# Optimization experiments

Measured on AMD Instinct MI355X. Metric: run time of the kernel, lower is better.

The kernel has to match this reference:

```python
import jax, jax.numpy as jnp
import numpy as np

B, L, D = 4096, 50, 64
NU, NI, NR = 100000, 100000, 5


def setup_inputs() -> dict:
    key = jax.random.key(0)
    ks = jax.random.split(key, 16)
    s = 0.02
    inp = {
        "nodes_v": jax.random.randint(ks[0], (B,), 0, NI),
        "neigh_u": jax.random.randint(ks[1], (B, L), 0, NU),
        "neigh_r": jax.random.randint(ks[2], (B, L), 0, NR),
        "embed_u": jax.random.normal(ks[3], (NU, D)) * s,
        "embed_i": jax.random.normal(ks[4], (NI, D)) * s,
        "embed_r": jax.random.normal(ks[5], (NR, D)) * s,
        # gv MLP: Linear(2D,D) ReLU Linear(D,D) ReLU Linear(D,D)
        "gv_w1": jax.random.normal(ks[6], (2 * D, D)) * s, "gv_b1": jnp.zeros((D,)),
        "gv_w2": jax.random.normal(ks[7], (D, D)) * s,     "gv_b2": jnp.zeros((D,)),
        "gv_w3": jax.random.normal(ks[8], (D, D)) * s,     "gv_b3": jnp.zeros((D,)),
        # attention MLP: Linear(2D,D) ReLU Linear(D,D) ReLU Linear(D,1), softmax over neighbors
        "att_w1": jax.random.normal(ks[9], (2 * D, D)) * s, "att_b1": jnp.zeros((D,)),
        "att_w2": jax.random.normal(ks[10], (D, D)) * s,    "att_b2": jnp.zeros((D,)),
        "att_w3": jax.random.normal(ks[11], (D, 1)) * s,    "att_b3": jnp.zeros((1,)),
        # combine: Linear(2D,D) ReLU Linear(D,D) ReLU
        "wr1_w": jax.random.normal(ks[12], (2 * D, D)) * s, "wr1_b": jnp.zeros((D,)),
        "wr2_w": jax.random.normal(ks[13], (D, D)) * s,     "wr2_b": jnp.zeros((D,)),
    }
    return inp


def reference(nodes_v, neigh_u, neigh_r, embed_u, embed_i, embed_r,
              gv_w1, gv_b1, gv_w2, gv_b2, gv_w3, gv_b3,
              att_w1, att_b1, att_w2, att_b2, att_w3, att_b3,
              wr1_w, wr1_b, wr2_w, wr2_b):
    qj = embed_i[nodes_v]            # [B, D] item reps
    pt = embed_u[neigh_u]            # [B, L, D] neighbor user reps
    er = embed_r[neigh_r]            # [B, L, D] rating reps
    # fusion MLP g(.)
    x = jnp.concatenate([pt, er], axis=-1)                    # [B, L, 2D]
    h = jax.nn.relu(x @ gv_w1 + gv_b1)
    h = jax.nn.relu(h @ gv_w2 + gv_b2)
    fjt = h @ gv_w3 + gv_b3                                   # [B, L, D]
    # attention over neighbors (dropout is identity in eval mode)
    q_rep = jnp.broadcast_to(qj[:, None, :], fjt.shape)       # [B, L, D]
    a = jnp.concatenate([fjt, q_rep], axis=-1)                # [B, L, 2D]
    a = jax.nn.relu(a @ att_w1 + att_b1)
    a = jax.nn.relu(a @ att_w2 + att_b2)
    scores = (a @ att_w3 + att_b3)[..., 0]                    # [B, L]
    mu = jax.nn.softmax(scores, axis=1)                       # softmax over neighbors
    zj = jnp.einsum("bld,bl->bd", fjt, mu)                   # weighted aggregation
    # combine aggregated neighborhood with item's own embedding (2D -> D)
    z = jax.nn.relu(jnp.concatenate([zj, qj], axis=-1) @ wr1_w + wr1_b)
    out = jax.nn.relu(z @ wr2_w + wr2_b)                      # [B, D]
    return out
```

## Files before the change

kernel.cpp:

```cpp
#include <hip/hip_runtime.h>

typedef __bf16 bf16;
typedef short s16x8 __attribute__((ext_vector_type(8)));
typedef __bf16 b16x8 __attribute__((ext_vector_type(8)));
typedef float f32x4 __attribute__((ext_vector_type(4)));

#define B_   4096
#define L_   50
#define SH   72

#define OFF_W1F  0
#define OFF_W2F  8192
#define OFF_W3F  12288
#define OFF_WCF  16384
#define OFF_A2F  20480
#define OFF_R1T  24576
#define OFF_R2T  32768
#define WT_TOTAL 36864
#define BIAS1P_BYTE 73728
#define CQ_BYTE     73984

#define PREP_W_BLOCKS 145
#define PREP_C_BLOCKS 1024

__device__ __forceinline__ unsigned short f2b(float f) {
    __bf16 h = (__bf16)f;
    return __builtin_bit_cast(unsigned short, h);
}
__device__ __forceinline__ unsigned pack2(float a, float b) {
    return (unsigned)f2b(a) | ((unsigned)f2b(b) << 16);
}
__device__ __forceinline__ s16x8 mkfrag(float4 a, float4 b) {
    union { s16x8 v; unsigned u[4]; } r;
    r.u[0] = pack2(a.x, a.y); r.u[1] = pack2(a.z, a.w);
    r.u[2] = pack2(b.x, b.y); r.u[3] = pack2(b.z, b.w);
    return r.v;
}
__device__ __forceinline__ f32x4 mfma16(s16x8 a, s16x8 b, f32x4 c) {
    return __builtin_amdgcn_mfma_f32_16x16x32_bf16(a, b, c, 0, 0, 0);
}

template<bool RELU>
__device__ __forceinline__ void dual_layer_lds(const bf16* A0, const bf16* A1,
                                               const bf16* __restrict__ Wf,
                                               const float* __restrict__ bias,
                                               bf16* O0, bf16* O1, int lane)
{
    const int m = lane & 15, quad = lane >> 4;
    f32x4 ac0[4] = {}, ac1[4] = {};
#pragma unroll
    for (int kt = 0; kt < 2; ++kt) {
        s16x8 a0 = *(const s16x8*)(A0 + m * SH + kt * 32 + quad * 8);
        s16x8 a1 = *(const s16x8*)(A1 + m * SH + kt * 32 + quad * 8);
#pragma unroll
        for (int nt = 0; nt < 4; ++nt) {
            s16x8 b = *(const s16x8*)(Wf + (kt * 4 + nt) * 512 + lane * 8);
            ac0[nt] = mfma16(a0, b, ac0[nt]);
            ac1[nt] = mfma16(a1, b, ac1[nt]);
        }
    }
#pragma unroll
    for (int nt = 0; nt < 4; ++nt) {
        int c = nt * 16 + m;
        float bv = bias[c];
#pragma unroll
        for (int r4 = 0; r4 < 4; ++r4) {
            float v0 = ac0[nt][r4] + bv, v1 = ac1[nt][r4] + bv;
            if (RELU) { v0 = fmaxf(v0, 0.f); v1 = fmaxf(v1, 0.f); }
            O0[(quad * 4 + r4) * SH + c] = (bf16)v0;
            O1[(quad * 4 + r4) * SH + c] = (bf16)v1;
        }
    }
}

extern "C" __global__ void prep_all(const float* __restrict__ w1, const float* __restrict__ w2,
                                    const float* __restrict__ w3, const float* __restrict__ a1,
                                    const float* __restrict__ a2, const float* __restrict__ r1,
                                    const float* __restrict__ r2, const float* __restrict__ gb3,
                                    const float* __restrict__ ab1,
                                    const int* __restrict__ nodes_v, const float* __restrict__ embed_i,
                                    bf16* __restrict__ wt, float* __restrict__ bias1p,
                                    float* __restrict__ cq)
{
    if (blockIdx.x >= PREP_W_BLOCKS) {
        int gid = (blockIdx.x - PREP_W_BLOCKS) * 256 + threadIdx.x;
        int b = gid >> 6, n = gid & 63;
        int v = nodes_v[b];
        const float* q = embed_i + v * 64;
        float s0 = 0.f, s1 = 0.f, s2 = 0.f, s3 = 0.f;
#pragma unroll
        for (int k = 0; k < 64; k += 4) {
            s0 = fmaf(q[k],     a1[(64 + k) * 64 + n],     s0);
            s1 = fmaf(q[k + 1], a1[(64 + k + 1) * 64 + n], s1);
            s2 = fmaf(q[k + 2], a1[(64 + k + 2) * 64 + n], s2);
            s3 = fmaf(q[k + 3], a1[(64 + k + 3) * 64 + n], s3);
        }
        cq[gid] = (s0 + s1) + (s2 + s3);
        return;
    }
    int i = blockIdx.x * 256 + threadIdx.x;
    if (i >= WT_TOTAL + 64) return;
    if (i >= WT_TOTAL) {
        int n = i - WT_TOTAL;
        float s0 = ab1[n], s1 = 0.f, s2 = 0.f, s3 = 0.f;
#pragma unroll
        for (int t = 0; t < 64; t += 4) {
            s0 = fmaf(gb3[t],     a1[t * 64 + n],       s0);
            s1 = fmaf(gb3[t + 1], a1[(t + 1) * 64 + n], s1);
            s2 = fmaf(gb3[t + 2], a1[(t + 2) * 64 + n], s2);
            s3 = fmaf(gb3[t + 3], a1[(t + 3) * 64 + n], s3);
        }
        bias1p[n] = (s0 + s1) + (s2 + s3);
        return;
    }
    float val;
    if (i < OFF_R1T) {
        int off, kind;
        if      (i < OFF_W2F) { off = OFF_W1F; kind = 0; }
        else if (i < OFF_W3F) { off = OFF_W2F; kind = 1; }
        else if (i < OFF_WCF) { off = OFF_W3F; kind = 2; }
        else if (i < OFF_A2F) { off = OFF_WCF; kind = 3; }
        else                  { off = OFF_A2F; kind = 4; }
        int local = i - off;
        int f = local >> 9, lane = (local >> 3) & 63, j = local & 7;
        int kt = f >> 2, nt = f & 3, quad = lane >> 4, m = lane & 15;
        int k = kt * 32 + quad * 8 + j;
        int n = nt * 16 + m;
        if (kind == 0)      val = w1[k * 64 + n];
        else if (kind == 1) val = w2[k * 64 + n];
        else if (kind == 2) val = w3[k * 64 + n];
        else if (kind == 4) val = a2[k * 64 + n];
        else {
            float s0 = 0.f, s1 = 0.f, s2 = 0.f, s3 = 0.f;
#pragma unroll
            for (int t = 0; t < 64; t += 4) {
                float4 w = *(const float4*)(w3 + k * 64 + t);
                s0 = fmaf(w.x, a1[t * 64 + n],       s0);
                s1 = fmaf(w.y, a1[(t + 1) * 64 + n], s1);
                s2 = fmaf(w.z, a1[(t + 2) * 64 + n], s2);
                s3 = fmaf(w.w, a1[(t + 3) * 64 + n], s3);
            }
            val = (s0 + s1) + (s2 + s3);
        }
    }
    else if (i < OFF_R2T) { int li = i - OFF_R1T; int n = li >> 7, k = li & 127; val = r1[k * 64 + n]; }
    else                  { int li = i - OFF_R2T; int n = li >> 6, k = li & 63;  val = r2[k * 64 + n]; }
    wt[i] = (bf16)val;
}

extern "C" __global__ void __launch_bounds__(256, 2)
dense_fused(const int* __restrict__ nodes_v, const int* __restrict__ neigh_u,
            const int* __restrict__ neigh_r,
            const float* __restrict__ embed_u, const float* __restrict__ embed_i,
            const float* __restrict__ embed_r,
            const float* __restrict__ gv_b1, const float* __restrict__ gv_b2,
            const float* __restrict__ gv_b3,
            const float* __restrict__ att_b2, const float* __restrict__ att_w3,
            const float* __restrict__ wr1_b, const float* __restrict__ wr2_b,
            const bf16* __restrict__ wt, const float* __restrict__ cq,
            const float* __restrict__ bias1p, float* __restrict__ out)
{
    __shared__ __align__(16) bf16 H[128 * SH];
    __shared__ float csS[128];
    __shared__ float qsh[128];
    __shared__ float scs[128];
    __shared__ float zp[4 * 64];

    const int tid = threadIdx.x;
    const int lane = tid & 63, wave = tid >> 6;
    const int m = lane & 15, quad = lane >> 4;
    const int b0 = blockIdx.x * 2;
    const int rw0 = wave * 32;
    const int item_w = rw0 >> 6;
    const int lbase = rw0 & 63;

    if (tid < 128) {
        int item = tid >> 6, n = tid & 63;
        csS[tid] = cq[(b0 + item) * 64 + n] + bias1p[n];
        qsh[tid] = embed_i[nodes_v[b0 + item] * 64 + n];
    }

    const int bw = b0 + item_w;
    const int l0 = min(lbase + m, L_ - 1);
    const int l1 = min(lbase + 16 + m, L_ - 1);
    const int u0 = neigh_u[bw * L_ + l0], u1 = neigh_u[bw * L_ + l1];
    const int v0 = neigh_r[bw * L_ + l0], v1 = neigh_r[bw * L_ + l1];

    bf16* Hw = H + rw0 * SH;
    bf16* H0 = Hw;
    bf16* H1 = Hw + 16 * SH;

    {
        const float* b00 = embed_u + u0 * 64;
        const float* b01 = embed_u + u1 * 64;
        const float* b10 = embed_r + v0 * 64;
        const float* b11 = embed_r + v1 * 64;
        f32x4 ac0[4] = {}, ac1[4] = {};
#pragma unroll
        for (int kt = 0; kt < 4; ++kt) {
            const float* s0p = (kt < 2 ? b00 : b10) + (kt & 1) * 32 + quad * 8;
            const float* s1p = (kt < 2 ? b01 : b11) + (kt & 1) * 32 + quad * 8;
            float4 a0a = *(const float4*)s0p, a0b = *(const float4*)(s0p + 4);
            float4 a1a = *(const float4*)s1p, a1b = *(const float4*)(s1p + 4);
            s16x8 a0 = mkfrag(a0a, a0b);
            s16x8 a1 = mkfrag(a1a, a1b);
#pragma unroll
            for (int nt = 0; nt < 4; ++nt) {
                s16x8 b = *(const s16x8*)(wt + OFF_W1F + (kt * 4 + nt) * 512 + lane * 8);
                ac0[nt] = mfma16(a0, b, ac0[nt]);
                ac1[nt] = mfma16(a1, b, ac1[nt]);
            }
        }
#pragma unroll
        for (int nt = 0; nt < 4; ++nt) {
            int c = nt * 16 + m;
            float bv = gv_b1[c];
#pragma unroll
            for (int r4 = 0; r4 < 4; ++r4) {
                H0[(quad * 4 + r4) * SH + c] = (bf16)fmaxf(ac0[nt][r4] + bv, 0.f);
                H1[(quad * 4 + r4) * SH + c] = (bf16)fmaxf(ac1[nt][r4] + bv, 0.f);
            }
        }
    }

    dual_layer_lds<true>(H0, H1, wt + OFF_W2F, gv_b2, H0, H1, lane);

    __syncthreads();

    f32x4 aF0[4] = {}, aF1[4] = {};
    {
        const bf16* w3f = wt + OFF_W3F;
        const bf16* wcf = wt + OFF_WCF;
        f32x4 aA0[4] = {}, aA1[4] = {};
#pragma unroll
        for (int kt = 0; kt < 2; ++kt) {
            s16x8 a0 = *(const s16x8*)(H0 + m * SH + kt * 32 + quad * 8);
            s16x8 a1 = *(const s16x8*)(H1 + m * SH + kt * 32 + quad * 8);
#pragma unroll
            for (int nt = 0; nt < 4; ++nt) {
                s16x8 bF = *(const s16x8*)(w3f + (kt * 4 + nt) * 512 + lane * 8);
                s16x8 bA = *(const s16x8*)(wcf + (kt * 4 + nt) * 512 + lane * 8);
                aF0[nt] = mfma16(a0, bF, aF0[nt]);
                aF1[nt] = mfma16(a1, bF, aF1[nt]);
                aA0[nt] = mfma16(a0, bA, aA0[nt]);
                aA1[nt] = mfma16(a1, bA, aA1[nt]);
            }
        }
#pragma unroll
        for (int nt = 0; nt < 4; ++nt) {
            int c = nt * 16 + m;
            float b1v = csS[item_w * 64 + c];
#pragma unroll
            for (int r4 = 0; r4 < 4; ++r4) {
                H0[(quad * 4 + r4) * SH + c] = (bf16)fmaxf(aA0[nt][r4] + b1v, 0.f);
                H1[(quad * 4 + r4) * SH + c] = (bf16)fmaxf(aA1[nt][r4] + b1v, 0.f);
            }
        }
    }

    {
        const bf16* a2f = wt + OFF_A2F;
        f32x4 ac0[4] = {}, ac1[4] = {};
#pragma unroll
        for (int kt = 0; kt < 2; ++kt) {
            s16x8 a0 = *(const s16x8*)(H0 + m * SH + kt * 32 + quad * 8);
            s16x8 a1 = *(const s16x8*)(H1 + m * SH + kt * 32 + quad * 8);
#pragma unroll
            for (int nt = 0; nt < 4; ++nt) {
                s16x8 b = *(const s16x8*)(a2f + (kt * 4 + nt) * 512 + lane * 8);
                ac0[nt] = mfma16(a0, b, ac0[nt]);
                ac1[nt] = mfma16(a1, b, ac1[nt]);
            }
        }
        float s0[4] = {0.f, 0.f, 0.f, 0.f}, s1[4] = {0.f, 0.f, 0.f, 0.f};
#pragma unroll
        for (int nt = 0; nt < 4; ++nt) {
            int c = nt * 16 + m;
            float b2v = att_b2[c], w3v = att_w3[c];
#pragma unroll
            for (int r4 = 0; r4 < 4; ++r4) {
                s0[r4] += fmaxf(ac0[nt][r4] + b2v, 0.f) * w3v;
                s1[r4] += fmaxf(ac1[nt][r4] + b2v, 0.f) * w3v;
            }
        }
#pragma unroll
        for (int mask = 1; mask < 16; mask <<= 1)
#pragma unroll
            for (int r4 = 0; r4 < 4; ++r4) {
                s0[r4] += __shfl_xor(s0[r4], mask);
                s1[r4] += __shfl_xor(s1[r4], mask);
            }
        if (m == 0) {
#pragma unroll
            for (int r4 = 0; r4 < 4; ++r4) {
                scs[item_w * 64 + lbase + quad * 4 + r4] = s0[r4];
                scs[item_w * 64 + lbase + 16 + quad * 4 + r4] = s1[r4];
            }
        }
    }
    __syncthreads();

    {
        float s = (lane < L_) ? scs[item_w * 64 + lane] : -1e30f;
        float mx = s;
#pragma unroll
        for (int off = 32; off; off >>= 1) mx = fmaxf(mx, __shfl_xor(mx, off));
        float e = (lane < L_) ? __expf(s - mx) : 0.f;
        float sum = e;
#pragma unroll
        for (int off = 32; off; off >>= 1) sum += __shfl_xor(sum, off);
        float mu = e / sum;

        float z[4] = {0.f, 0.f, 0.f, 0.f};
#pragma unroll
        for (int r4 = 0; r4 < 4; ++r4) {
            float m0 = __shfl(mu, lbase + quad * 4 + r4);
            float m1 = __shfl(mu, lbase + 16 + quad * 4 + r4);
#pragma unroll
            for (int nt = 0; nt < 4; ++nt)
                z[nt] += aF0[nt][r4] * m0 + aF1[nt][r4] * m1;
        }
#pragma unroll
        for (int nt = 0; nt < 4; ++nt) {
            z[nt] += __shfl_xor(z[nt], 16);
            z[nt] += __shfl_xor(z[nt], 32);
        }
        if (quad == 0) {
#pragma unroll
            for (int nt = 0; nt < 4; ++nt) zp[wave * 64 + nt * 16 + m] = z[nt];
        }
    }
    __syncthreads();

    if ((wave & 1) == 0) {
        const int item = wave >> 1;
        const int d = lane;
        float z = zp[wave * 64 + d] + zp[wave * 64 + 64 + d] + gv_b3[d];
        float* zsh = scs + item * 64;
        zsh[d] = z;

        float accz = wr1_b[d];
        const bf16* r1 = wt + OFF_R1T + d * 128;
#pragma unroll
        for (int k8 = 0; k8 < 8; ++k8) {
            b16x8 wv = *(const b16x8*)(r1 + k8 * 8);
#pragma unroll
            for (int j = 0; j < 8; ++j) accz = fmaf((float)wv[j], zsh[k8 * 8 + j], accz);
        }
#pragma unroll
        for (int k8 = 0; k8 < 8; ++k8) {
            b16x8 wv = *(const b16x8*)(r1 + 64 + k8 * 8);
#pragma unroll
            for (int j = 0; j < 8; ++j) accz = fmaf((float)wv[j], qsh[item * 64 + k8 * 8 + j], accz);
        }
        float* z2sh = zp + wave * 64;
        z2sh[d] = fmaxf(accz, 0.f);

        float acco = wr2_b[d];
        const bf16* r2 = wt + OFF_R2T + d * 64;
#pragma unroll
        for (int k8 = 0; k8 < 8; ++k8) {
            b16x8 wv = *(const b16x8*)(r2 + k8 * 8);
#pragma unroll
            for (int j = 0; j < 8; ++j) acco = fmaf((float)wv[j], z2sh[k8 * 8 + j], acco);
        }
        out[(b0 + item) * 64 + d] = fmaxf(acco, 0.f);
    }
}

extern "C" void kernel_launch(void* const* d_in, const int* in_sizes, int n_in,
                              void* d_out, int out_size, void* d_ws, size_t ws_size,
                              hipStream_t stream)
{
    const int* nodes_v = (const int*)d_in[0];
    const int* neigh_u = (const int*)d_in[1];
    const int* neigh_r = (const int*)d_in[2];
    const float* embed_u = (const float*)d_in[3];
    const float* embed_i = (const float*)d_in[4];
    const float* embed_r = (const float*)d_in[5];
    const float* gv_w1  = (const float*)d_in[6];  const float* gv_b1 = (const float*)d_in[7];
    const float* gv_w2  = (const float*)d_in[8];  const float* gv_b2 = (const float*)d_in[9];
    const float* gv_w3  = (const float*)d_in[10]; const float* gv_b3 = (const float*)d_in[11];
    const float* att_w1 = (const float*)d_in[12]; const float* att_b1 = (const float*)d_in[13];
    const float* att_w2 = (const float*)d_in[14]; const float* att_b2 = (const float*)d_in[15];
    const float* att_w3 = (const float*)d_in[16]; const float* att_b3 = (const float*)d_in[17];
    const float* wr1_w  = (const float*)d_in[18]; const float* wr1_b = (const float*)d_in[19];
    const float* wr2_w  = (const float*)d_in[20]; const float* wr2_b = (const float*)d_in[21];
    (void)att_b3;

    bf16*  wt     = (bf16*)d_ws;
    float* bias1p = (float*)((char*)d_ws + BIAS1P_BYTE);
    float* cq     = (float*)((char*)d_ws + CQ_BYTE);

    prep_all<<<PREP_W_BLOCKS + PREP_C_BLOCKS, 256, 0, stream>>>(
        gv_w1, gv_w2, gv_w3, att_w1, att_w2, wr1_w, wr2_w, gv_b3, att_b1,
        nodes_v, embed_i, wt, bias1p, cq);
    dense_fused<<<B_ / 2, 256, 0, stream>>>(nodes_v, neigh_u, neigh_r,
                                            embed_u, embed_i, embed_r,
                                            gv_b1, gv_b2, gv_b3, att_b2, att_w3,
                                            wr1_b, wr2_b, wt, cq, bias1p, (float*)d_out);
}
```

Measured before the change: 169.3 us.

## Process one batch item per block with one 16-row tile per wave

```diff
diff --git a/kernel.cpp b/kernel.cpp
--- a/kernel.cpp
+++ b/kernel.cpp
@@ -38,39 +38,6 @@
 }
 __device__ __forceinline__ f32x4 mfma16(s16x8 a, s16x8 b, f32x4 c) {
     return __builtin_amdgcn_mfma_f32_16x16x32_bf16(a, b, c, 0, 0, 0);
-}
-
-template<bool RELU>
-__device__ __forceinline__ void dual_layer_lds(const bf16* A0, const bf16* A1,
-                                               const bf16* __restrict__ Wf,
-                                               const float* __restrict__ bias,
-                                               bf16* O0, bf16* O1, int lane)
-{
-    const int m = lane & 15, quad = lane >> 4;
-    f32x4 ac0[4] = {}, ac1[4] = {};
-#pragma unroll
-    for (int kt = 0; kt < 2; ++kt) {
-        s16x8 a0 = *(const s16x8*)(A0 + m * SH + kt * 32 + quad * 8);
-        s16x8 a1 = *(const s16x8*)(A1 + m * SH + kt * 32 + quad * 8);
-#pragma unroll
-        for (int nt = 0; nt < 4; ++nt) {
-            s16x8 b = *(const s16x8*)(Wf + (kt * 4 + nt) * 512 + lane * 8);
-            ac0[nt] = mfma16(a0, b, ac0[nt]);
-            ac1[nt] = mfma16(a1, b, ac1[nt]);
-        }
-    }
-#pragma unroll
-    for (int nt = 0; nt < 4; ++nt) {
-        int c = nt * 16 + m;
-        float bv = bias[c];
-#pragma unroll
-        for (int r4 = 0; r4 < 4; ++r4) {
-            float v0 = ac0[nt][r4] + bv, v1 = ac1[nt][r4] + bv;
-            if (RELU) { v0 = fmaxf(v0, 0.f); v1 = fmaxf(v1, 0.f); }
-            O0[(quad * 4 + r4) * SH + c] = (bf16)v0;
-            O1[(quad * 4 + r4) * SH + c] = (bf16)v1;
-        }
-    }
 }
 
 extern "C" __global__ void prep_all(const float* __restrict__ w1, const float* __restrict__ w2,
@@ -160,55 +127,39 @@
             const bf16* __restrict__ wt, const float* __restrict__ cq,
             const float* __restrict__ bias1p, float* __restrict__ out)
 {
-    __shared__ __align__(16) bf16 H[128 * SH];
-    __shared__ float csS[128];
-    __shared__ float qsh[128];
-    __shared__ float scs[128];
+    __shared__ __align__(16) bf16 H[64 * SH];
+    __shared__ float csS[64];
+    __shared__ float qsh[64];
+    __shared__ float scs[64];
     __shared__ float zp[4 * 64];
 
     const int tid = threadIdx.x;
     const int lane = tid & 63, wave = tid >> 6;
     const int m = lane & 15, quad = lane >> 4;
-    const int b0 = blockIdx.x * 2;
-    const int rw0 = wave * 32;
-    const int item_w = rw0 >> 6;
-    const int lbase = rw0 & 63;
-
-    if (tid < 128) {
-        int item = tid >> 6, n = tid & 63;
-        csS[tid] = cq[(b0 + item) * 64 + n] + bias1p[n];
-        qsh[tid] = embed_i[nodes_v[b0 + item] * 64 + n];
-    }
-
-    const int bw = b0 + item_w;
-    const int l0 = min(lbase + m, L_ - 1);
-    const int l1 = min(lbase + 16 + m, L_ - 1);
-    const int u0 = neigh_u[bw * L_ + l0], u1 = neigh_u[bw * L_ + l1];
-    const int v0 = neigh_r[bw * L_ + l0], v1 = neigh_r[bw * L_ + l1];
-
-    bf16* Hw = H + rw0 * SH;
-    bf16* H0 = Hw;
-    bf16* H1 = Hw + 16 * SH;
-
-    {
-        const float* b00 = embed_u + u0 * 64;
-        const float* b01 = embed_u + u1 * 64;
-        const float* b10 = embed_r + v0 * 64;
-        const float* b11 = embed_r + v1 * 64;
-        f32x4 ac0[4] = {}, ac1[4] = {};
+    const int b = blockIdx.x;
+
+    if (tid < 64)        csS[tid] = cq[b * 64 + tid] + bias1p[tid];
+    else if (tid < 128)  qsh[tid - 64] = embed_i[nodes_v[b] * 64 + (tid - 64)];
+
+    const int l = min(wave * 16 + m, L_ - 1);
+    const int u = neigh_u[b * L_ + l];
+    const int r = neigh_r[b * L_ + l];
+
+    bf16* Hw = H + wave * 16 * SH;
+
+    {
+        const float* pu = embed_u + u * 64;
+        const float* pr = embed_r + r * 64;
+        f32x4 ac[4] = {};
 #pragma unroll
         for (int kt = 0; kt < 4; ++kt) {
-            const float* s0p = (kt < 2 ? b00 : b10) + (kt & 1) * 32 + quad * 8;
-            const float* s1p = (kt < 2 ? b01 : b11) + (kt & 1) * 32 + quad * 8;
-            float4 a0a = *(const float4*)s0p, a0b = *(const float4*)(s0p + 4);
-            float4 a1a = *(const float4*)s1p, a1b = *(const float4*)(s1p + 4);
-            s16x8 a0 = mkfrag(a0a, a0b);
-            s16x8 a1 = mkfrag(a1a, a1b);
+            const float* sp = (kt < 2 ? pu : pr) + (kt & 1) * 32 + quad * 8;
+            float4 aa = *(const float4*)sp, ab = *(const float4*)(sp + 4);
+            s16x8 af = mkfrag(aa, ab);
 #pragma unroll
             for (int nt = 0; nt < 4; ++nt) {
-                s16x8 b = *(const s16x8*)(wt + OFF_W1F + (kt * 4 + nt) * 512 + lane * 8);
-                ac0[nt] = mfma16(a0, b, ac0[nt]);
-                ac1[nt] = mfma16(a1, b, ac1[nt]);
+                s16x8 bw = *(const s16x8*)(wt + OFF_W1F + (kt * 4 + nt) * 512 + lane * 8);
+                ac[nt] = mfma16(af, bw, ac[nt]);
             }
         }
 #pragma unroll
@@ -216,92 +167,92 @@
             int c = nt * 16 + m;
             float bv = gv_b1[c];
 #pragma unroll
-            for (int r4 = 0; r4 < 4; ++r4) {
-                H0[(quad * 4 + r4) * SH + c] = (bf16)fmaxf(ac0[nt][r4] + bv, 0.f);
-                H1[(quad * 4 + r4) * SH + c] = (bf16)fmaxf(ac1[nt][r4] + bv, 0.f);
-            }
-        }
-    }
-
-    dual_layer_lds<true>(H0, H1, wt + OFF_W2F, gv_b2, H0, H1, lane);
+            for (int r4 = 0; r4 < 4; ++r4)
+                Hw[(quad * 4 + r4) * SH + c] = (bf16)fmaxf(ac[nt][r4] + bv, 0.f);
+        }
+    }
+
+    {
+        f32x4 ac[4] = {};
+#pragma unroll
+        for (int kt = 0; kt < 2; ++kt) {
+            s16x8 a = *(const s16x8*)(Hw + m * SH + kt * 32 + quad * 8);
+#pragma unroll
+            for (int nt = 0; nt < 4; ++nt) {
+                s16x8 bw = *(const s16x8*)(wt + OFF_W2F + (kt * 4 + nt) * 512 + lane * 8);
+                ac[nt] = mfma16(a, bw, ac[nt]);
+            }
+        }
+#pragma unroll
+        for (int nt = 0; nt < 4; ++nt) {
+            int c = nt * 16 + m;
+            float bv = gv_b2[c];
+#pragma unroll
+            for (int r4 = 0; r4 < 4; ++r4)
+                Hw[(quad * 4 + r4) * SH + c] = (bf16)fmaxf(ac[nt][r4] + bv, 0.f);
+        }
+    }
 
     __syncthreads();
 
-    f32x4 aF0[4] = {}, aF1[4] = {};
-    {
-        const bf16* w3f = wt + OFF_W3F;
-        const bf16* wcf = wt + OFF_WCF;
-        f32x4 aA0[4] = {}, aA1[4] = {};
+    f32x4 aF[4] = {};
+    {
+        f32x4 aA[4] = {};
 #pragma unroll
         for (int kt = 0; kt < 2; ++kt) {
-            s16x8 a0 = *(const s16x8*)(H0 + m * SH + kt * 32 + quad * 8);
-            s16x8 a1 = *(const s16x8*)(H1 + m * SH + kt * 32 + quad * 8);
+            s16x8 a = *(const s16x8*)(Hw + m * SH + kt * 32 + quad * 8);
 #pragma unroll
             for (int nt = 0; nt < 4; ++nt) {
-                s16x8 bF = *(const s16x8*)(w3f + (kt * 4 + nt) * 512 + lane * 8);
-                s16x8 bA = *(const s16x8*)(wcf + (kt * 4 + nt) * 512 + lane * 8);
-                aF0[nt] = mfma16(a0, bF, aF0[nt]);
-                aF1[nt] = mfma16(a1, bF, aF1[nt]);
-                aA0[nt] = mfma16(a0, bA, aA0[nt]);
-                aA1[nt] = mfma16(a1, bA, aA1[nt]);
+                s16x8 bF = *(const s16x8*)(wt + OFF_W3F + (kt * 4 + nt) * 512 + lane * 8);
+                s16x8 bA = *(const s16x8*)(wt + OFF_WCF + (kt * 4 + nt) * 512 + lane * 8);
+                aF[nt] = mfma16(a, bF, aF[nt]);
+                aA[nt] = mfma16(a, bA, aA[nt]);
             }
         }
 #pragma unroll
         for (int nt = 0; nt < 4; ++nt) {
             int c = nt * 16 + m;
-            float b1v = csS[item_w * 64 + c];
-#pragma unroll
-            for (int r4 = 0; r4 < 4; ++r4) {
-                H0[(quad * 4 + r4) * SH + c] = (bf16)fmaxf(aA0[nt][r4] + b1v, 0.f);
-                H1[(quad * 4 + r4) * SH + c] = (bf16)fmaxf(aA1[nt][r4] + b1v, 0.f);
-            }
-        }
-    }
-
-    {
-        const bf16* a2f = wt + OFF_A2F;
-        f32x4 ac0[4] = {}, ac1[4] = {};
+            float b1v = csS[c];
+#pragma unroll
+            for (int r4 = 0; r4 < 4; ++r4)
+                Hw[(quad * 4 + r4) * SH + c] = (bf16)fmaxf(aA[nt][r4] + b1v, 0.f);
+        }
+    }
+
+    {
+        f32x4 ac[4] = {};
 #pragma unroll
         for (int kt = 0; kt < 2; ++kt) {
-            s16x8 a0 = *(const s16x8*)(H0 + m * SH + kt * 32 + quad * 8);
-            s16x8 a1 = *(const s16x8*)(H1 + m * SH + kt * 32 + quad * 8);
+            s16x8 a = *(const s16x8*)(Hw + m * SH + kt * 32 + quad * 8);
 #pragma unroll
             for (int nt = 0; nt < 4; ++nt) {
-                s16x8 b = *(const s16x8*)(a2f + (kt * 4 + nt) * 512 + lane * 8);
-                ac0[nt] = mfma16(a0, b, ac0[nt]);
-                ac1[nt] = mfma16(a1, b, ac1[nt]);
-            }
-        }
-        float s0[4] = {0.f, 0.f, 0.f, 0.f}, s1[4] = {0.f, 0.f, 0.f, 0.f};
+                s16x8 bw = *(const s16x8*)(wt + OFF_A2F + (kt * 4 + nt) * 512 + lane * 8);
+                ac[nt] = mfma16(a, bw, ac[nt]);
+            }
+        }
+        float sc[4] = {0.f, 0.f, 0.f, 0.f};
 #pragma unroll
         for (int nt = 0; nt < 4; ++nt) {
             int c = nt * 16 + m;
             float b2v = att_b2[c], w3v = att_w3[c];
 #pragma unroll
-            for (int r4 = 0; r4 < 4; ++r4) {
-                s0[r4] += fmaxf(ac0[nt][r4] + b2v, 0.f) * w3v;
-                s1[r4] += fmaxf(ac1[nt][r4] + b2v, 0.f) * w3v;
-            }
+            for (int r4 = 0; r4 < 4; ++r4)
+                sc[r4] += fmaxf(ac[nt][r4] + b2v, 0.f) * w3v;
         }
 #pragma unroll
         for (int mask = 1; mask < 16; mask <<= 1)
 #pragma unroll
-            for (int r4 = 0; r4 < 4; ++r4) {
-                s0[r4] += __shfl_xor(s0[r4], mask);
-                s1[r4] += __shfl_xor(s1[r4], mask);
-            }
+            for (int r4 = 0; r4 < 4; ++r4) sc[r4] += __shfl_xor(sc[r4], mask);
         if (m == 0) {
 #pragma unroll
-            for (int r4 = 0; r4 < 4; ++r4) {
-                scs[item_w * 64 + lbase + quad * 4 + r4] = s0[r4];
-                scs[item_w * 64 + lbase + 16 + quad * 4 + r4] = s1[r4];
-            }
+            for (int r4 = 0; r4 < 4; ++r4)
+                scs[wave * 16 + quad * 4 + r4] = sc[r4];
         }
     }
     __syncthreads();
 
     {
-        float s = (lane < L_) ? scs[item_w * 64 + lane] : -1e30f;
+        float s = (lane < L_) ? scs[lane] : -1e30f;
         float mx = s;
 #pragma unroll
         for (int off = 32; off; off >>= 1) mx = fmaxf(mx, __shfl_xor(mx, off));
@@ -314,11 +265,9 @@
         float z[4] = {0.f, 0.f, 0.f, 0.f};
 #pragma unroll
         for (int r4 = 0; r4 < 4; ++r4) {
-            float m0 = __shfl(mu, lbase + quad * 4 + r4);
-            float m1 = __shfl(mu, lbase + 16 + quad * 4 + r4);
-#pragma unroll
-            for (int nt = 0; nt < 4; ++nt)
-                z[nt] += aF0[nt][r4] * m0 + aF1[nt][r4] * m1;
+            float mr = __shfl(mu, wave * 16 + quad * 4 + r4);
+#pragma unroll
+            for (int nt = 0; nt < 4; ++nt) z[nt] += aF[nt][r4] * mr;
         }
 #pragma unroll
         for (int nt = 0; nt < 4; ++nt) {
@@ -332,12 +281,10 @@
     }
     __syncthreads();
 
-    if ((wave & 1) == 0) {
-        const int item = wave >> 1;
+    if (wave == 0) {
         const int d = lane;
-        float z = zp[wave * 64 + d] + zp[wave * 64 + 64 + d] + gv_b3[d];
-        float* zsh = scs + item * 64;
-        zsh[d] = z;
+        float z = zp[d] + zp[64 + d] + zp[128 + d] + zp[192 + d] + gv_b3[d];
+        scs[d] = z;
 
         float accz = wr1_b[d];
         const bf16* r1 = wt + OFF_R1T + d * 128;
@@ -345,16 +292,15 @@
         for (int k8 = 0; k8 < 8; ++k8) {
             b16x8 wv = *(const b16x8*)(r1 + k8 * 8);
 #pragma unroll
-            for (int j = 0; j < 8; ++j) accz = fmaf((float)wv[j], zsh[k8 * 8 + j], accz);
+            for (int j = 0; j < 8; ++j) accz = fmaf((float)wv[j], scs[k8 * 8 + j], accz);
         }
 #pragma unroll
         for (int k8 = 0; k8 < 8; ++k8) {
             b16x8 wv = *(const b16x8*)(r1 + 64 + k8 * 8);
 #pragma unroll
-            for (int j = 0; j < 8; ++j) accz = fmaf((float)wv[j], qsh[item * 64 + k8 * 8 + j], accz);
-        }
-        float* z2sh = zp + wave * 64;
-        z2sh[d] = fmaxf(accz, 0.f);
+            for (int j = 0; j < 8; ++j) accz = fmaf((float)wv[j], qsh[k8 * 8 + j], accz);
+        }
+        zp[d] = fmaxf(accz, 0.f);
 
         float acco = wr2_b[d];
         const bf16* r2 = wt + OFF_R2T + d * 64;
@@ -362,9 +308,9 @@
         for (int k8 = 0; k8 < 8; ++k8) {
             b16x8 wv = *(const b16x8*)(r2 + k8 * 8);
 #pragma unroll
-            for (int j = 0; j < 8; ++j) acco = fmaf((float)wv[j], z2sh[k8 * 8 + j], acco);
-        }
-        out[(b0 + item) * 64 + d] = fmaxf(acco, 0.f);
+            for (int j = 0; j < 8; ++j) acco = fmaf((float)wv[j], zp[k8 * 8 + j], acco);
+        }
+        out[b * 64 + d] = fmaxf(acco, 0.f);
     }
 }
 
@@ -395,8 +341,8 @@
     prep_all<<<PREP_W_BLOCKS + PREP_C_BLOCKS, 256, 0, stream>>>(
         gv_w1, gv_w2, gv_w3, att_w1, att_w2, wr1_w, wr2_w, gv_b3, att_b1,
         nodes_v, embed_i, wt, bias1p, cq);
-    dense_fused<<<B_ / 2, 256, 0, stream>>>(nodes_v, neigh_u, neigh_r,
-                                            embed_u, embed_i, embed_r,
-                                            gv_b1, gv_b2, gv_b3, att_b2, att_w3,
-                                            wr1_b, wr2_b, wt, cq, bias1p, (float*)d_out);
-}
+    dense_fused<<<B_, 256, 0, stream>>>(nodes_v, neigh_u, neigh_r,
+                                        embed_u, embed_i, embed_r,
+                                        gv_b1, gv_b2, gv_b3, att_b2, att_w3,
+                                        wr1_b, wr2_b, wt, cq, bias1p, (float*)d_out);
+}
```

Measured after the change: 174.9 us. 1.03x slower.
